# Optimization experiments

Hardware: AMD Instinct MI355X
Metric: run time of the kernel (lower is better)

Reference implementation:

```python
import jax, jax.numpy as jnp
import numpy as np

N = 50000
NEG_SLOPE = 0.2

def gat_conv(x, src, dst, W, a_src, a_dst, bias, heads, out_ch):
    # Linear projection per head: [N, H, C]
    h = (x @ W).reshape(x.shape[0], heads, out_ch)
    # Node-level attention terms alpha_src/alpha_dst: [N, H]
    al_src = jnp.einsum('nhc,hc->nh', h, a_src)
    al_dst = jnp.einsum('nhc,hc->nh', h, a_dst)
    # Edge logits with LeakyReLU: [E, H]
    logits = jax.nn.leaky_relu(al_src[src] + al_dst[dst], NEG_SLOPE)
    # Segment softmax over incoming edges of each dst node
    m = jax.ops.segment_max(logits, dst, num_segments=N)
    e = jnp.exp(logits - m[dst])
    s = jax.ops.segment_sum(e, dst, num_segments=N)
    alpha = e / (s[dst] + 1e-16)                      # [E, H]
    # Weighted message aggregation (scatter-add): [N, H, C]
    out = jax.ops.segment_sum(h[src] * alpha[..., None], dst, num_segments=N)
    return out.reshape(N, heads * out_ch) + bias


def setup_inputs() -> dict:
    key = jax.random.key(0)
    ks = jax.random.split(key, 12)
    in_ch, out_ch = 128, 256
    h1, c1 = 4, out_ch // 8          # conv1: 4 heads x 32
    mid = h1 * c1                    # 128 = out_ch // 2
    E = 1600000
    x = jax.random.normal(ks[0], (N, in_ch), jnp.float32)
    edge_index = jax.random.randint(ks[1], (2, E), 0, N, jnp.int64)
    sc = 0.1
    return {
        'x': x,
        'edge_index': edge_index,
        'W1': jax.random.normal(ks[2], (in_ch, h1 * c1), jnp.float32) * sc,
        'a_src1': jax.random.normal(ks[3], (h1, c1), jnp.float32) * sc,
        'a_dst1': jax.random.normal(ks[4], (h1, c1), jnp.float32) * sc,
        'b1': jnp.zeros((h1 * c1,), jnp.float32),
        'W2': jax.random.normal(ks[5], (mid, out_ch), jnp.float32) * sc,
        'a_src2': jax.random.normal(ks[6], (1, out_ch), jnp.float32) * sc,
        'a_dst2': jax.random.normal(ks[7], (1, out_ch), jnp.float32) * sc,
        'b2': jnp.zeros((out_ch,), jnp.float32),
    }


def reference(x, edge_index, W1, a_src1, a_dst1, b1, W2, a_src2, a_dst2, b2):
    # PyG GATConv adds self-loops by default
    loop = jnp.arange(N, dtype=edge_index.dtype)
    src = jnp.concatenate([edge_index[0], loop])
    dst = jnp.concatenate([edge_index[1], loop])
    h = gat_conv(x, src, dst, W1, a_src1, a_dst1, b1, heads=4, out_ch=32)
    h = jax.nn.relu(h)
    out = gat_conv(h, src, dst, W2, a_src2, a_dst2, b2, heads=1, out_ch=256)
    return out
```

## Files before the change

### kernel.cpp

```cpp
#include <hip/hip_runtime.h>
#include <hip/hip_fp16.h>
#include <math.h>

#define NSLOPE 0.2f
#define LOG2E  1.44269504f

typedef _Float16 half8 __attribute__((ext_vector_type(8)));
typedef float floatx4 __attribute__((ext_vector_type(4)));
typedef float floatx2 __attribute__((ext_vector_type(2)));

__device__ __forceinline__ float wcalc(float t) {
    float l = fmaxf(t, NSLOPE * t);
    float r;
    asm("v_exp_f32 %0, %1" : "=v"(r) : "v"(l));
    return r;
}

__device__ __forceinline__ void fma8_fp8(float* acc, float w, uint2 v) {
    floatx2 p0 = __builtin_amdgcn_cvt_pk_f32_fp8(v.x, false);
    floatx2 p1 = __builtin_amdgcn_cvt_pk_f32_fp8(v.x, true);
    floatx2 p2 = __builtin_amdgcn_cvt_pk_f32_fp8(v.y, false);
    floatx2 p3 = __builtin_amdgcn_cvt_pk_f32_fp8(v.y, true);
    acc[0] = fmaf(w, p0.x, acc[0]);
    acc[1] = fmaf(w, p0.y, acc[1]);
    acc[2] = fmaf(w, p1.x, acc[2]);
    acc[3] = fmaf(w, p1.y, acc[3]);
    acc[4] = fmaf(w, p2.x, acc[4]);
    acc[5] = fmaf(w, p2.y, acc[5]);
    acc[6] = fmaf(w, p3.x, acc[6]);
    acc[7] = fmaf(w, p3.y, acc[7]);
}

#define MAXB 5632
#define BE   8192

__global__ __launch_bounds__(256)
void prep_kernel(const int* __restrict__ dst, int* __restrict__ bcnt,
                 const float* __restrict__ x, __half* __restrict__ x16, int nx,
                 const float* __restrict__ W1, __half* __restrict__ W1T,
                 const float* __restrict__ W2, __half* __restrict__ W2T,
                 const float* __restrict__ a_src2, const float* __restrict__ a_dst2,
                 float* __restrict__ w2s, float* __restrict__ w2d,
                 int E, int Etot, int nb, int nbA, int ncast, int nt1, int nt2)
{
    __shared__ int hist[512];
    int bid = blockIdx.x;
    int tid = threadIdx.x;

    if (bid < nbA) {
        for (int i = tid; i < 512; i += 256) hist[i] = 0;
        __syncthreads();
        for (int e = bid * 256 + tid; e < Etot; e += nbA * 256) {
            int d = (e < E) ? dst[e] : (e - E);
            atomicAdd(&hist[d >> 7], 1);
        }
        __syncthreads();
        for (int i = tid; i < nb; i += 256) {
            int v = hist[i];
            if (v) atomicAdd(&bcnt[i], v);
        }
        return;
    }
    bid -= nbA;
    if (bid < ncast) {
        int i = (bid * 256 + tid) * 4;
        if (i < nx) {
            float4 v = *(const float4*)&x[i];
            __half2 a = __floats2half2_rn(v.x, v.y);
            __half2 b = __floats2half2_rn(v.z, v.w);
            *(uint2*)&x16[i] = make_uint2(*(unsigned*)&a, *(unsigned*)&b);
        }
        return;
    }
    bid -= ncast;
    if (bid < nt1) {
        int idx = bid * 256 + tid;
        int c = idx >> 7, k = idx & 127;
        W1T[(size_t)c * 128 + k] = __float2half(W1[(size_t)k * 128 + c]);
        return;
    }
    bid -= nt1;
    if (bid < nt2) {
        int idx = bid * 256 + tid;
        int c = idx >> 7, k = idx & 127;
        W2T[(size_t)c * 128 + k] = __float2half(W2[(size_t)k * 256 + c]);
        return;
    }
    {
        const float* a = (tid < 128) ? a_src2 : a_dst2;
        int k = tid & 127;
        float acc = 0.f;
        for (int c = 0; c < 256; c += 4) {
            float4 w = *(const float4*)&W2[(size_t)k * 256 + c];
            float4 av = *(const float4*)&a[c];
            acc = fmaf(w.x, av.x, fmaf(w.y, av.y, fmaf(w.z, av.z, fmaf(w.w, av.w, acc))));
        }
        if (tid < 128) w2s[k] = acc * LOG2E; else w2d[k] = acc * LOG2E;
    }
}

__global__ __launch_bounds__(512)
void scanBuckets_kernel(const int* __restrict__ bcnt, int* __restrict__ bbase,
                        int* __restrict__ gcur, int nb, int* __restrict__ offs,
                        int N, int total)
{
    __shared__ int tmp[512];
    int tid = threadIdx.x;
    int v = (tid < nb) ? bcnt[tid] : 0;
    tmp[tid] = v;
    __syncthreads();
    for (int off = 1; off < 512; off <<= 1) {
        int t = (tid >= off) ? tmp[tid - off] : 0;
        __syncthreads();
        tmp[tid] += t;
        __syncthreads();
    }
    if (tid < nb) {
        int e = tmp[tid] - v;
        bbase[tid] = e;
        gcur[tid] = e;
    }
    if (tid == 0) offs[N] = total;
}

__global__ __launch_bounds__(256)
void bucketB_kernel(const int* __restrict__ src, const int* __restrict__ dst,
                    int* __restrict__ gcur, unsigned* __restrict__ eout,
                    int E, int Etot, int nb)
{
    __shared__ int hist[512];
    __shared__ int res[512];
    __shared__ int lcur[512];
    int tid = threadIdx.x;
    int e0 = blockIdx.x * BE;
    int e1 = min(e0 + BE, Etot);

    for (int i = tid; i < 512; i += 256) hist[i] = 0;
    __syncthreads();
    for (int e = e0 + tid; e < e1; e += 256) {
        int d = (e < E) ? dst[e] : (e - E);
        atomicAdd(&hist[d >> 7], 1);
    }
    __syncthreads();
    for (int i = tid; i < nb; i += 256) {
        int h = hist[i];
        res[i] = h ? atomicAdd(&gcur[i], h) : 0;
        lcur[i] = 0;
    }
    __syncthreads();
    for (int e = e0 + tid; e < e1; e += 256) {
        int s, d;
        if (e < E) { s = src[e]; d = dst[e]; }
        else       { s = e - E; d = s; }
        int b = d >> 7;
        int p = res[b] + atomicAdd(&lcur[b], 1);
        eout[p] = (unsigned)s | ((unsigned)(d & 127) << 16);
    }
}

__global__ __launch_bounds__(256)
void combo_kernel(const unsigned* __restrict__ eout, const int* __restrict__ bbase,
                  const int* __restrict__ bcnt, unsigned short* __restrict__ csr,
                  int* __restrict__ offs, int N, int nb,
                  const __half* __restrict__ A16, const __half* __restrict__ W1T,
                  const float* __restrict__ a_src, const float* __restrict__ a_dst,
                  unsigned char* __restrict__ h1A, unsigned char* __restrict__ h1B,
                  float* __restrict__ al_src, float* __restrict__ al_dst)
{
    __shared__ unsigned eb[MAXB];
    __shared__ unsigned short sbuf[MAXB];
    __shared__ int cnt128[128], cur128[128], sc[128];

    int tid = threadIdx.x;
    if ((int)blockIdx.x < nb) {
        int b = blockIdx.x;
        int ebase = bbase[b];
        int ecnt = bcnt[b];
        int n0 = b << 7;
        int ncount = min(128, N - n0);

        if (tid < 128) cnt128[tid] = 0;
        for (int i = tid; i < ecnt; i += 256) eb[i] = eout[ebase + i];
        __syncthreads();
        for (int i = tid; i < ecnt; i += 256) atomicAdd(&cnt128[eb[i] >> 16], 1);
        __syncthreads();
        if (tid < 128) sc[tid] = cnt128[tid];
        __syncthreads();
        for (int off = 1; off < 128; off <<= 1) {
            int t = (tid >= off && tid < 128) ? sc[tid - off] : 0;
            __syncthreads();
            if (tid < 128) sc[tid] += t;
            __syncthreads();
        }
        if (tid < 128) {
            int excl = sc[tid] - cnt128[tid];
            cur128[tid] = excl;
            if (tid < ncount) offs[n0 + tid] = ebase + excl;
        }
        __syncthreads();
        for (int i = tid; i < ecnt; i += 256) {
            unsigned v = eb[i];
            int p = atomicAdd(&cur128[v >> 16], 1);
            sbuf[p] = (unsigned short)(v & 0xFFFFu);
        }
        __syncthreads();
        for (int i = tid; i < ecnt; i += 256) csr[ebase + i] = sbuf[i];
        return;
    }

    int gb = blockIdx.x - nb;
    int M = N;
    int wave = tid >> 6, lane = tid & 63;
    int lr = lane & 15, q = lane >> 4;
    int r0 = gb * 32 + (wave >> 1) * 16;
    int wcol = (wave & 1) * 64;
    unsigned char* hT = (wave & 1) ? h1B : h1A;

    int arow = min(r0 + lr, M - 1);
    const uint4* Arow = (const uint4*)A16 + (size_t)arow * 16;
    half8 a[4];
#pragma unroll
    for (int kb = 0; kb < 4; ++kb) {
        union { uint4 u; half8 h; } c;
        c.u = Arow[kb * 4 + q];
        a[kb] = c.h;
    }

    floatx4 acc[4];
    const floatx4 zero = {0.f, 0.f, 0.f, 0.f};
#pragma unroll
    for (int ct = 0; ct < 4; ++ct) acc[ct] = zero;

#pragma unroll
    for (int ct = 0; ct < 4; ++ct) {
        const uint4* Brow = (const uint4*)W1T + (size_t)(wcol + ct * 16 + lr) * 16;
#pragma unroll
        for (int kb = 0; kb < 4; ++kb) {
            union { uint4 u; half8 h; } c;
            c.u = Brow[kb * 4 + q];
            acc[ct] = __builtin_amdgcn_mfma_f32_16x16x32_f16(a[kb], c.h, acc[ct], 0, 0, 0);
        }
    }

#pragma unroll
    for (int ct = 0; ct < 4; ++ct) {
        int colh = ct * 16 + lr;
#pragma unroll
        for (int r = 0; r < 4; ++r) {
            int row = r0 + q * 4 + r;
            if (row < M) {
                unsigned pk = __builtin_amdgcn_cvt_pk_fp8_f32(acc[ct][r], acc[ct][r], 0, false);
                hT[(size_t)row * 64 + colh] = (unsigned char)(pk & 0xFF);
            }
        }
    }

    float as[4], ad[4];
#pragma unroll
    for (int ct = 0; ct < 4; ++ct) {
        int col = wcol + ct * 16 + lr;
        as[ct] = a_src[col] * LOG2E;
        ad[ct] = a_dst[col] * LOG2E;
    }
    int hb = wcol >> 5;
#pragma unroll
    for (int r = 0; r < 4; ++r) {
        float psA = acc[0][r] * as[0] + acc[1][r] * as[1];
        float psB = acc[2][r] * as[2] + acc[3][r] * as[3];
        float pdA = acc[0][r] * ad[0] + acc[1][r] * ad[1];
        float pdB = acc[2][r] * ad[2] + acc[3][r] * ad[3];
#pragma unroll
        for (int off = 1; off < 16; off <<= 1) {
            psA += __shfl_xor(psA, off); psB += __shfl_xor(psB, off);
            pdA += __shfl_xor(pdA, off); pdB += __shfl_xor(pdB, off);
        }
        if (lr == 0) {
            int row = r0 + q * 4 + r;
            if (row < M) {
                al_src[(size_t)row * 4 + hb]     = psA;
                al_src[(size_t)row * 4 + hb + 1] = psB;
                al_dst[(size_t)row * 4 + hb]     = pdA;
                al_dst[(size_t)row * 4 + hb + 1] = pdB;
            }
        }
    }
}

__global__ __launch_bounds__(256)
void gemm2_mfma(const __half* __restrict__ A16, const __half* __restrict__ W2T,
                const float* __restrict__ bias, float* __restrict__ out, int M)
{
    int wave = threadIdx.x >> 6, lane = threadIdx.x & 63;
    int lr = lane & 15, q = lane >> 4;
    int r0 = blockIdx.x * 16;
    int c0 = wave * 64;

    int arow = min(r0 + lr, M - 1);
    const uint4* Arow = (const uint4*)A16 + (size_t)arow * 16;
    half8 a[4];
#pragma unroll
    for (int kb = 0; kb < 4; ++kb) {
        union { uint4 u; half8 h; } c;
        c.u = Arow[kb * 4 + q];
        a[kb] = c.h;
    }

    floatx4 acc[4];
    const floatx4 zero = {0.f, 0.f, 0.f, 0.f};
#pragma unroll
    for (int ct = 0; ct < 4; ++ct) acc[ct] = zero;

#pragma unroll
    for (int ct = 0; ct < 4; ++ct) {
        const uint4* Brow = (const uint4*)W2T + (size_t)(c0 + ct * 16 + lr) * 16;
#pragma unroll
        for (int kb = 0; kb < 4; ++kb) {
            union { uint4 u; half8 h; } c;
            c.u = Brow[kb * 4 + q];
            acc[ct] = __builtin_amdgcn_mfma_f32_16x16x32_f16(a[kb], c.h, acc[ct], 0, 0, 0);
        }
    }

#pragma unroll
    for (int ct = 0; ct < 4; ++ct) {
        int col = c0 + ct * 16 + lr;
        float b = bias[col];
#pragma unroll
        for (int r = 0; r < 4; ++r) {
            int row = r0 + q * 4 + r;
            if (row < M) out[(size_t)row * 256 + col] = acc[ct][r] + b;
        }
    }
}

__global__ __launch_bounds__(256)
void agg1_half_kernel(const unsigned char* __restrict__ feat,
                      const unsigned short* __restrict__ csr_src,
                      const int* __restrict__ offs, const float* __restrict__ alS,
                      const float* __restrict__ alD, const float* __restrict__ bias,
                      const float* __restrict__ w2s, const float* __restrict__ w2d,
                      unsigned char* __restrict__ hmidH, float* __restrict__ alS2,
                      float* __restrict__ alD2, int N, int half)
{
    int lane = threadIdx.x & 63;
    int n = blockIdx.x * 4 + (threadIdx.x >> 6);
    if (n >= N) return;

    int lc = lane & 7;
    int es = lane >> 3;
    int head = half * 2 + (lc >> 2);

    float aD = alD[(size_t)n * 4 + head];
    int beg = offs[n], end = offs[n + 1];

    float acc0[8] = {0,0,0,0,0,0,0,0}, acc1[8] = {0,0,0,0,0,0,0,0};
    float sw0 = 0.f, sw1 = 0.f;
    const char* fbase = (const char*)feat + lc * 8;
    const float* alSh = alS + head;

    int j = beg + es;
    for (; j + 8 < end; j += 16) {
        int s0 = csr_src[j];
        int s1 = csr_src[j + 8];
        float w0 = wcalc(alSh[(size_t)s0 * 4] + aD);
        float w1 = wcalc(alSh[(size_t)s1 * 4] + aD);
        uint2 f0 = *(const uint2*)(fbase + (size_t)s0 * 64);
        uint2 f1 = *(const uint2*)(fbase + (size_t)s1 * 64);
        fma8_fp8(acc0, w0, f0); sw0 += w0;
        fma8_fp8(acc1, w1, f1); sw1 += w1;
    }
    if (j < end) {
        int s0 = csr_src[j];
        float w0 = wcalc(alSh[(size_t)s0 * 4] + aD);
        uint2 f0 = *(const uint2*)(fbase + (size_t)s0 * 64);
        fma8_fp8(acc0, w0, f0); sw0 += w0;
    }

    float sw = sw0 + sw1;
    sw += __shfl_xor(sw, 8); sw += __shfl_xor(sw, 16); sw += __shfl_xor(sw, 32);
#pragma unroll
    for (int i = 0; i < 8; ++i) {
        acc0[i] += acc1[i];
        acc0[i] += __shfl_xor(acc0[i], 8);
        acc0[i] += __shfl_xor(acc0[i], 16);
        acc0[i] += __shfl_xor(acc0[i], 32);
    }

    if (lane < 8) {
        float inv = 1.f / (sw + 1e-16f);
        int cb = half * 64 + lc * 8;
        float v[8];
#pragma unroll
        for (int i = 0; i < 8; ++i)
            v[i] = fmaxf(fmaf(acc0[i], inv, bias[cb + i]), 0.f);
        unsigned pk0 = __builtin_amdgcn_cvt_pk_fp8_f32(v[0], v[1], 0, false);
        pk0 = __builtin_amdgcn_cvt_pk_fp8_f32(v[2], v[3], pk0, true);
        unsigned pk1 = __builtin_amdgcn_cvt_pk_fp8_f32(v[4], v[5], 0, false);
        pk1 = __builtin_amdgcn_cvt_pk_fp8_f32(v[6], v[7], pk1, true);
        ((uint2*)hmidH)[(size_t)n * 8 + lc] = make_uint2(pk0, pk1);
        float ps = 0.f, pd = 0.f;
#pragma unroll
        for (int i = 0; i < 8; ++i) {
            ps = fmaf(v[i], w2s[cb + i], ps);
            pd = fmaf(v[i], w2d[cb + i], pd);
        }
        ps += __shfl_xor(ps, 1); ps += __shfl_xor(ps, 2); ps += __shfl_xor(ps, 4);
        pd += __shfl_xor(pd, 1); pd += __shfl_xor(pd, 2); pd += __shfl_xor(pd, 4);
        if (lane == 0) {
            if (half == 0) { alS2[n] = ps;          alD2[n] = pd; }
            else           { alS2[n] = alS2[n] + ps; alD2[n] = alD2[n] + pd; }
        }
    }
}

__global__ __launch_bounds__(256)
void agg2_half_kernel(const unsigned char* __restrict__ feat,
                      const unsigned short* __restrict__ csr_src,
                      const int* __restrict__ offs, const float* __restrict__ alS,
                      const float* __restrict__ alD, __half* __restrict__ m16,
                      int N, int half)
{
    int lane = threadIdx.x & 63;
    int n = blockIdx.x * 4 + (threadIdx.x >> 6);
    if (n >= N) return;

    int lc = lane & 7;
    int es = lane >> 3;

    float aD = alD[n];
    int beg = offs[n], end = offs[n + 1];

    float acc0[8] = {0,0,0,0,0,0,0,0}, acc1[8] = {0,0,0,0,0,0,0,0};
    float sw0 = 0.f, sw1 = 0.f;
    const char* fbase = (const char*)feat + lc * 8;

    int j = beg + es;
    for (; j + 8 < end; j += 16) {
        int s0 = csr_src[j];
        int s1 = csr_src[j + 8];
        float w0 = wcalc(alS[s0] + aD);
        float w1 = wcalc(alS[s1] + aD);
        uint2 f0 = *(const uint2*)(fbase + (size_t)s0 * 64);
        uint2 f1 = *(const uint2*)(fbase + (size_t)s1 * 64);
        fma8_fp8(acc0, w0, f0); sw0 += w0;
        fma8_fp8(acc1, w1, f1); sw1 += w1;
    }
    if (j < end) {
        int s0 = csr_src[j];
        float w0 = wcalc(alS[s0] + aD);
        uint2 f0 = *(const uint2*)(fbase + (size_t)s0 * 64);
        fma8_fp8(acc0, w0, f0); sw0 += w0;
    }

    float sw = sw0 + sw1;
    sw += __shfl_xor(sw, 8); sw += __shfl_xor(sw, 16); sw += __shfl_xor(sw, 32);
#pragma unroll
    for (int i = 0; i < 8; ++i) {
        acc0[i] += acc1[i];
        acc0[i] += __shfl_xor(acc0[i], 8);
        acc0[i] += __shfl_xor(acc0[i], 16);
        acc0[i] += __shfl_xor(acc0[i], 32);
    }

    if (lane < 8) {
        float inv = 1.f / (sw + 1e-16f);
        float v[8];
#pragma unroll
        for (int i = 0; i < 8; ++i) v[i] = acc0[i] * inv;
        __half2 p0 = __floats2half2_rn(v[0], v[1]);
        __half2 p1 = __floats2half2_rn(v[2], v[3]);
        __half2 p2 = __floats2half2_rn(v[4], v[5]);
        __half2 p3 = __floats2half2_rn(v[6], v[7]);
        uint4 pk = make_uint4(*(unsigned*)&p0, *(unsigned*)&p1,
                              *(unsigned*)&p2, *(unsigned*)&p3);
        ((uint4*)m16)[(size_t)n * 16 + half * 8 + lc] = pk;
    }
}

extern "C" void kernel_launch(void* const* d_in, const int* in_sizes, int n_in,
                              void* d_out, int out_size, void* d_ws, size_t ws_size,
                              hipStream_t stream)
{
    const float* x      = (const float*)d_in[0];
    const int*   ei     = (const int*)d_in[1];
    const float* W1     = (const float*)d_in[2];
    const float* a_src1 = (const float*)d_in[3];
    const float* a_dst1 = (const float*)d_in[4];
    const float* b1     = (const float*)d_in[5];
    const float* W2     = (const float*)d_in[6];
    const float* a_src2 = (const float*)d_in[7];
    const float* a_dst2 = (const float*)d_in[8];
    const float* b2     = (const float*)d_in[9];

    const int N    = in_sizes[0] / 128;
    const int E    = in_sizes[1] / 2;
    const int Etot = E + N;
    const int* src = ei;
    const int* dst = ei + E;
    const int nb   = (N + 127) >> 7;

    char* ws = (char*)d_ws;
    size_t off = 0;
    auto carve = [&](size_t bytes) -> void* {
        void* p = ws + off;
        off += (bytes + 255) & ~(size_t)255;
        return p;
    };
    __half*  x16  = (__half*)carve((size_t)N * 128 * 2);
    unsigned char* h1A   = (unsigned char*)carve((size_t)N * 64);
    unsigned char* h1B   = (unsigned char*)carve((size_t)N * 64);
    unsigned char* hmidA = (unsigned char*)carve((size_t)N * 64);
    unsigned char* hmidB = (unsigned char*)carve((size_t)N * 64);
    __half*  m16  = (__half*)carve((size_t)N * 128 * 2);
    __half*  W1T  = (__half*)carve(128 * 128 * 2);
    __half*  W2T  = (__half*)carve(256 * 128 * 2);
    float*   alS1 = (float*)carve((size_t)N * 4 * 4);
    float*   alD1 = (float*)carve((size_t)N * 4 * 4);
    float*   alS2 = (float*)carve((size_t)N * 4);
    float*   alD2 = (float*)carve((size_t)N * 4);
    float*   w2s  = (float*)carve(128 * 4);
    float*   w2d  = (float*)carve(128 * 4);
    int*     offs = (int*)carve((size_t)(N + 1) * 4);
    int*     bcnt = (int*)carve(512 * 4);
    int*     bbas = (int*)carve(512 * 4);
    int*     gcur = (int*)carve(512 * 4);
    unsigned* eout = (unsigned*)carve((size_t)Etot * 4);
    unsigned short* csr = (unsigned short*)carve((size_t)Etot * 2);
    (void)ws_size; (void)n_in; (void)out_size;

    const int TB = 256;
    const int agrid = (N + 3) / 4;
    const int g1grid = (N + 31) / 32;
    const int g2grid = (N + 15) / 16;
    const int nx = N * 128;

    const int nbA   = 512;
    const int ncast = (nx / 4 + TB - 1) / TB;
    const int nt1   = (128 * 128 + TB - 1) / TB;
    const int nt2   = (256 * 128 + TB - 1) / TB;
    const int nprep = nbA + ncast + nt1 + nt2 + 1;

    hipMemsetAsync(bcnt, 0, 512 * 4, stream);

    prep_kernel<<<nprep, TB, 0, stream>>>(dst, bcnt, x, x16, nx, W1, W1T, W2, W2T,
                                          a_src2, a_dst2, w2s, w2d,
                                          E, Etot, nb, nbA, ncast, nt1, nt2);
    scanBuckets_kernel<<<1, 512, 0, stream>>>(bcnt, bbas, gcur, nb, offs, N, Etot);
    bucketB_kernel<<<(Etot + BE - 1) / BE, TB, 0, stream>>>(src, dst, gcur, eout, E, Etot, nb);
    combo_kernel<<<nb + g1grid, TB, 0, stream>>>(eout, bbas, bcnt, csr, offs, N, nb,
                                                 x16, W1T, a_src1, a_dst1, h1A, h1B, alS1, alD1);
    agg1_half_kernel<<<agrid, TB, 0, stream>>>(h1A, csr, offs, alS1, alD1, b1,
                                               w2s, w2d, hmidA, alS2, alD2, N, 0);
    agg1_half_kernel<<<agrid, TB, 0, stream>>>(h1B, csr, offs, alS1, alD1, b1,
                                               w2s, w2d, hmidB, alS2, alD2, N, 1);
    agg2_half_kernel<<<agrid, TB, 0, stream>>>(hmidA, csr, offs, alS2, alD2, m16, N, 0);
    agg2_half_kernel<<<agrid, TB, 0, stream>>>(hmidB, csr, offs, alS2, alD2, m16, N, 1);
    gemm2_mfma<<<g2grid, TB, 0, stream>>>(m16, W2T, b2, (float*)d_out, N);
}
```

Before: 336.8 us.

## Merge half-split fp8 feature buffers and aggregate full rows in one pass

Replaces the two half-width fp8 feature buffers (64 bytes per node) with single 128-byte rows. Each aggregation layer now runs as one kernel instead of two, with each lane loading 16 bytes per edge and accumulating with packed FMA. This halves the number of times the CSR, offsets and attention scalars are traversed and removes the read-modify-write of alS2/alD2 across halves. In exchange it uses more accumulator registers per lane, which may lower occupancy, and issues wider gathers.

```diff
diff --git a/kernel.cpp b/kernel.cpp
--- a/kernel.cpp
+++ b/kernel.cpp
@@ -16,19 +16,16 @@
     return r;
 }
 
-__device__ __forceinline__ void fma8_fp8(float* acc, float w, uint2 v) {
-    floatx2 p0 = __builtin_amdgcn_cvt_pk_f32_fp8(v.x, false);
-    floatx2 p1 = __builtin_amdgcn_cvt_pk_f32_fp8(v.x, true);
-    floatx2 p2 = __builtin_amdgcn_cvt_pk_f32_fp8(v.y, false);
-    floatx2 p3 = __builtin_amdgcn_cvt_pk_f32_fp8(v.y, true);
-    acc[0] = fmaf(w, p0.x, acc[0]);
-    acc[1] = fmaf(w, p0.y, acc[1]);
-    acc[2] = fmaf(w, p1.x, acc[2]);
-    acc[3] = fmaf(w, p1.y, acc[3]);
-    acc[4] = fmaf(w, p2.x, acc[4]);
-    acc[5] = fmaf(w, p2.y, acc[5]);
-    acc[6] = fmaf(w, p3.x, acc[6]);
-    acc[7] = fmaf(w, p3.y, acc[7]);
+__device__ __forceinline__ void fma16_fp8(floatx2* acc, float w, uint4 v) {
+    floatx2 ww; ww.x = w; ww.y = w;
+    unsigned u[4] = {v.x, v.y, v.z, v.w};
+#pragma unroll
+    for (int i = 0; i < 4; ++i) {
+        floatx2 lo = __builtin_amdgcn_cvt_pk_f32_fp8(u[i], false);
+        floatx2 hi = __builtin_amdgcn_cvt_pk_f32_fp8(u[i], true);
+        asm("v_pk_fma_f32 %0, %1, %2, %0" : "+v"(acc[2 * i])     : "v"(lo), "v"(ww));
+        asm("v_pk_fma_f32 %0, %1, %2, %0" : "+v"(acc[2 * i + 1]) : "v"(hi), "v"(ww));
+    }
 }
 
 #define MAXB 5632
@@ -164,8 +161,8 @@
                   int* __restrict__ offs, int N, int nb,
                   const __half* __restrict__ A16, const __half* __restrict__ W1T,
                   const float* __restrict__ a_src, const float* __restrict__ a_dst,
-                  unsigned char* __restrict__ h1A, unsigned char* __restrict__ h1B,
-                  float* __restrict__ al_src, float* __restrict__ al_dst)
+                  unsigned char* __restrict__ h1, float* __restrict__ al_src,
+                  float* __restrict__ al_dst)
 {
     __shared__ unsigned eb[MAXB];
     __shared__ unsigned short sbuf[MAXB];
@@ -214,7 +211,6 @@
     int lr = lane & 15, q = lane >> 4;
     int r0 = gb * 32 + (wave >> 1) * 16;
     int wcol = (wave & 1) * 64;
-    unsigned char* hT = (wave & 1) ? h1B : h1A;
 
     int arow = min(r0 + lr, M - 1);
     const uint4* Arow = (const uint4*)A16 + (size_t)arow * 16;
@@ -244,13 +240,13 @@
 
 #pragma unroll
     for (int ct = 0; ct < 4; ++ct) {
-        int colh = ct * 16 + lr;
+        int col = wcol + ct * 16 + lr;
 #pragma unroll
         for (int r = 0; r < 4; ++r) {
             int row = r0 + q * 4 + r;
             if (row < M) {
                 unsigned pk = __builtin_amdgcn_cvt_pk_fp8_f32(acc[ct][r], acc[ct][r], 0, false);
-                hT[(size_t)row * 64 + colh] = (unsigned char)(pk & 0xFF);
+                h1[(size_t)row * 128 + col] = (unsigned char)(pk & 0xFF);
             }
         }
     }
@@ -334,13 +330,12 @@
 }
 
 __global__ __launch_bounds__(256)
-void agg1_half_kernel(const unsigned char* __restrict__ feat,
-                      const unsigned short* __restrict__ csr_src,
-                      const int* __restrict__ offs, const float* __restrict__ alS,
-                      const float* __restrict__ alD, const float* __restrict__ bias,
-                      const float* __restrict__ w2s, const float* __restrict__ w2d,
-                      unsigned char* __restrict__ hmidH, float* __restrict__ alS2,
-                      float* __restrict__ alD2, int N, int half)
+void agg1_kernel(const unsigned char* __restrict__ feat, const unsigned short* __restrict__ csr_src,
+                 const int* __restrict__ offs, const float* __restrict__ alS,
+                 const float* __restrict__ alD, const float* __restrict__ bias,
+                 const float* __restrict__ w2s, const float* __restrict__ w2d,
+                 unsigned char* __restrict__ hmid, float* __restrict__ alS2,
+                 float* __restrict__ alD2, int N)
 {
     int lane = threadIdx.x & 63;
     int n = blockIdx.x * 4 + (threadIdx.x >> 6);
@@ -348,77 +343,79 @@
 
     int lc = lane & 7;
     int es = lane >> 3;
-    int head = half * 2 + (lc >> 2);
-
-    float aD = alD[(size_t)n * 4 + head];
+    int head = lc >> 1;
+    unsigned lcoff = (unsigned)(lc * 16);
+
+    float aD = alD[(unsigned)(n << 2) + head];
     int beg = offs[n], end = offs[n + 1];
 
-    float acc0[8] = {0,0,0,0,0,0,0,0}, acc1[8] = {0,0,0,0,0,0,0,0};
+    floatx2 acc0[8], acc1[8];
+    floatx2 zz; zz.x = 0.f; zz.y = 0.f;
+#pragma unroll
+    for (int i = 0; i < 8; ++i) { acc0[i] = zz; acc1[i] = zz; }
     float sw0 = 0.f, sw1 = 0.f;
-    const char* fbase = (const char*)feat + lc * 8;
-    const float* alSh = alS + head;
 
     int j = beg + es;
     for (; j + 8 < end; j += 16) {
         int s0 = csr_src[j];
         int s1 = csr_src[j + 8];
-        float w0 = wcalc(alSh[(size_t)s0 * 4] + aD);
-        float w1 = wcalc(alSh[(size_t)s1 * 4] + aD);
-        uint2 f0 = *(const uint2*)(fbase + (size_t)s0 * 64);
-        uint2 f1 = *(const uint2*)(fbase + (size_t)s1 * 64);
-        fma8_fp8(acc0, w0, f0); sw0 += w0;
-        fma8_fp8(acc1, w1, f1); sw1 += w1;
+        float w0 = wcalc(alS[(unsigned)(s0 << 2) + head] + aD);
+        float w1 = wcalc(alS[(unsigned)(s1 << 2) + head] + aD);
+        uint4 f0 = *(const uint4*)(feat + ((unsigned)(s0 << 7) + lcoff));
+        uint4 f1 = *(const uint4*)(feat + ((unsigned)(s1 << 7) + lcoff));
+        fma16_fp8(acc0, w0, f0); sw0 += w0;
+        fma16_fp8(acc1, w1, f1); sw1 += w1;
     }
     if (j < end) {
         int s0 = csr_src[j];
-        float w0 = wcalc(alSh[(size_t)s0 * 4] + aD);
-        uint2 f0 = *(const uint2*)(fbase + (size_t)s0 * 64);
-        fma8_fp8(acc0, w0, f0); sw0 += w0;
+        float w0 = wcalc(alS[(unsigned)(s0 << 2) + head] + aD);
+        uint4 f0 = *(const uint4*)(feat + ((unsigned)(s0 << 7) + lcoff));
+        fma16_fp8(acc0, w0, f0); sw0 += w0;
     }
 
     float sw = sw0 + sw1;
     sw += __shfl_xor(sw, 8); sw += __shfl_xor(sw, 16); sw += __shfl_xor(sw, 32);
+    float v[16];
 #pragma unroll
     for (int i = 0; i < 8; ++i) {
-        acc0[i] += acc1[i];
-        acc0[i] += __shfl_xor(acc0[i], 8);
-        acc0[i] += __shfl_xor(acc0[i], 16);
-        acc0[i] += __shfl_xor(acc0[i], 32);
-    }
-
+        float e0 = acc0[i].x + acc1[i].x;
+        float e1 = acc0[i].y + acc1[i].y;
+        e0 += __shfl_xor(e0, 8); e0 += __shfl_xor(e0, 16); e0 += __shfl_xor(e0, 32);
+        e1 += __shfl_xor(e1, 8); e1 += __shfl_xor(e1, 16); e1 += __shfl_xor(e1, 32);
+        v[2 * i] = e0; v[2 * i + 1] = e1;
+    }
+
+    float ps = 0.f, pd = 0.f;
     if (lane < 8) {
         float inv = 1.f / (sw + 1e-16f);
-        int cb = half * 64 + lc * 8;
-        float v[8];
-#pragma unroll
-        for (int i = 0; i < 8; ++i)
-            v[i] = fmaxf(fmaf(acc0[i], inv, bias[cb + i]), 0.f);
-        unsigned pk0 = __builtin_amdgcn_cvt_pk_fp8_f32(v[0], v[1], 0, false);
-        pk0 = __builtin_amdgcn_cvt_pk_fp8_f32(v[2], v[3], pk0, true);
-        unsigned pk1 = __builtin_amdgcn_cvt_pk_fp8_f32(v[4], v[5], 0, false);
-        pk1 = __builtin_amdgcn_cvt_pk_fp8_f32(v[6], v[7], pk1, true);
-        ((uint2*)hmidH)[(size_t)n * 8 + lc] = make_uint2(pk0, pk1);
-        float ps = 0.f, pd = 0.f;
-#pragma unroll
-        for (int i = 0; i < 8; ++i) {
+        int cb = lc * 16;
+#pragma unroll
+        for (int i = 0; i < 16; ++i)
+            v[i] = fmaxf(fmaf(v[i], inv, bias[cb + i]), 0.f);
+        unsigned q0 = __builtin_amdgcn_cvt_pk_fp8_f32(v[0],  v[1],  0, false);
+        q0 = __builtin_amdgcn_cvt_pk_fp8_f32(v[2],  v[3],  q0, true);
+        unsigned q1 = __builtin_amdgcn_cvt_pk_fp8_f32(v[4],  v[5],  0, false);
+        q1 = __builtin_amdgcn_cvt_pk_fp8_f32(v[6],  v[7],  q1, true);
+        unsigned q2 = __builtin_amdgcn_cvt_pk_fp8_f32(v[8],  v[9],  0, false);
+        q2 = __builtin_amdgcn_cvt_pk_fp8_f32(v[10], v[11], q2, true);
+        unsigned q3 = __builtin_amdgcn_cvt_pk_fp8_f32(v[12], v[13], 0, false);
+        q3 = __builtin_amdgcn_cvt_pk_fp8_f32(v[14], v[15], q3, true);
+        ((uint4*)hmid)[(size_t)n * 8 + lc] = make_uint4(q0, q1, q2, q3);
+#pragma unroll
+        for (int i = 0; i < 16; ++i) {
             ps = fmaf(v[i], w2s[cb + i], ps);
             pd = fmaf(v[i], w2d[cb + i], pd);
         }
-        ps += __shfl_xor(ps, 1); ps += __shfl_xor(ps, 2); ps += __shfl_xor(ps, 4);
-        pd += __shfl_xor(pd, 1); pd += __shfl_xor(pd, 2); pd += __shfl_xor(pd, 4);
-        if (lane == 0) {
-            if (half == 0) { alS2[n] = ps;          alD2[n] = pd; }
-            else           { alS2[n] = alS2[n] + ps; alD2[n] = alD2[n] + pd; }
-        }
-    }
+    }
+    ps += __shfl_xor(ps, 1); ps += __shfl_xor(ps, 2); ps += __shfl_xor(ps, 4);
+    pd += __shfl_xor(pd, 1); pd += __shfl_xor(pd, 2); pd += __shfl_xor(pd, 4);
+    if (lane == 0) { alS2[n] = ps; alD2[n] = pd; }
 }
 
 __global__ __launch_bounds__(256)
-void agg2_half_kernel(const unsigned char* __restrict__ feat,
-                      const unsigned short* __restrict__ csr_src,
-                      const int* __restrict__ offs, const float* __restrict__ alS,
-                      const float* __restrict__ alD, __half* __restrict__ m16,
-                      int N, int half)
+void agg2_kernel(const unsigned char* __restrict__ feat, const unsigned short* __restrict__ csr_src,
+                 const int* __restrict__ offs, const float* __restrict__ alS,
+                 const float* __restrict__ alD, __half* __restrict__ m16, int N)
 {
     int lane = threadIdx.x & 63;
     int n = blockIdx.x * 4 + (threadIdx.x >> 6);
@@ -426,13 +423,16 @@
 
     int lc = lane & 7;
     int es = lane >> 3;
+    unsigned lcoff = (unsigned)(lc * 16);
 
     float aD = alD[n];
     int beg = offs[n], end = offs[n + 1];
 
-    float acc0[8] = {0,0,0,0,0,0,0,0}, acc1[8] = {0,0,0,0,0,0,0,0};
+    floatx2 acc0[8], acc1[8];
+    floatx2 zz; zz.x = 0.f; zz.y = 0.f;
+#pragma unroll
+    for (int i = 0; i < 8; ++i) { acc0[i] = zz; acc1[i] = zz; }
     float sw0 = 0.f, sw1 = 0.f;
-    const char* fbase = (const char*)feat + lc * 8;
 
     int j = beg + es;
     for (; j + 8 < end; j += 16) {
@@ -440,40 +440,42 @@
         int s1 = csr_src[j + 8];
         float w0 = wcalc(alS[s0] + aD);
         float w1 = wcalc(alS[s1] + aD);
-        uint2 f0 = *(const uint2*)(fbase + (size_t)s0 * 64);
-        uint2 f1 = *(const uint2*)(fbase + (size_t)s1 * 64);
-        fma8_fp8(acc0, w0, f0); sw0 += w0;
-        fma8_fp8(acc1, w1, f1); sw1 += w1;
+        uint4 f0 = *(const uint4*)(feat + ((unsigned)(s0 << 7) + lcoff));
+        uint4 f1 = *(const uint4*)(feat + ((unsigned)(s1 << 7) + lcoff));
+        fma16_fp8(acc0, w0, f0); sw0 += w0;
+        fma16_fp8(acc1, w1, f1); sw1 += w1;
     }
     if (j < end) {
         int s0 = csr_src[j];
         float w0 = wcalc(alS[s0] + aD);
-        uint2 f0 = *(const uint2*)(fbase + (size_t)s0 * 64);
-        fma8_fp8(acc0, w0, f0); sw0 += w0;
+        uint4 f0 = *(const uint4*)(feat + ((unsigned)(s0 << 7) + lcoff));
+        fma16_fp8(acc0, w0, f0); sw0 += w0;
     }
 
     float sw = sw0 + sw1;
     sw += __shfl_xor(sw, 8); sw += __shfl_xor(sw, 16); sw += __shfl_xor(sw, 32);
+    float v[16];
 #pragma unroll
     for (int i = 0; i < 8; ++i) {
-        acc0[i] += acc1[i];
-        acc0[i] += __shfl_xor(acc0[i], 8);
-        acc0[i] += __shfl_xor(acc0[i], 16);
-        acc0[i] += __shfl_xor(acc0[i], 32);
+        float e0 = acc0[i].x + acc1[i].x;
+        float e1 = acc0[i].y + acc1[i].y;
+        e0 += __shfl_xor(e0, 8); e0 += __shfl_xor(e0, 16); e0 += __shfl_xor(e0, 32);
+        e1 += __shfl_xor(e1, 8); e1 += __shfl_xor(e1, 16); e1 += __shfl_xor(e1, 32);
+        v[2 * i] = e0; v[2 * i + 1] = e1;
     }
 
     if (lane < 8) {
         float inv = 1.f / (sw + 1e-16f);
-        float v[8];
-#pragma unroll
-        for (int i = 0; i < 8; ++i) v[i] = acc0[i] * inv;
-        __half2 p0 = __floats2half2_rn(v[0], v[1]);
-        __half2 p1 = __floats2half2_rn(v[2], v[3]);
-        __half2 p2 = __floats2half2_rn(v[4], v[5]);
-        __half2 p3 = __floats2half2_rn(v[6], v[7]);
-        uint4 pk = make_uint4(*(unsigned*)&p0, *(unsigned*)&p1,
-                              *(unsigned*)&p2, *(unsigned*)&p3);
-        ((uint4*)m16)[(size_t)n * 16 + half * 8 + lc] = pk;
+        __half2 p[8];
+#pragma unroll
+        for (int i = 0; i < 8; ++i)
+            p[i] = __floats2half2_rn(v[2 * i] * inv, v[2 * i + 1] * inv);
+        uint4 pk0 = make_uint4(*(unsigned*)&p[0], *(unsigned*)&p[1],
+                               *(unsigned*)&p[2], *(unsigned*)&p[3]);
+        uint4 pk1 = make_uint4(*(unsigned*)&p[4], *(unsigned*)&p[5],
+                               *(unsigned*)&p[6], *(unsigned*)&p[7]);
+        ((uint4*)m16)[(size_t)n * 16 + lc * 2]     = pk0;
+        ((uint4*)m16)[(size_t)n * 16 + lc * 2 + 1] = pk1;
     }
 }
 
@@ -507,10 +509,8 @@
         return p;
     };
     __half*  x16  = (__half*)carve((size_t)N * 128 * 2);
-    unsigned char* h1A   = (unsigned char*)carve((size_t)N * 64);
-    unsigned char* h1B   = (unsigned char*)carve((size_t)N * 64);
-    unsigned char* hmidA = (unsigned char*)carve((size_t)N * 64);
-    unsigned char* hmidB = (unsigned char*)carve((size_t)N * 64);
+    unsigned char* h1   = (unsigned char*)carve((size_t)N * 128);
+    unsigned char* hmid = (unsigned char*)carve((size_t)N * 128);
     __half*  m16  = (__half*)carve((size_t)N * 128 * 2);
     __half*  W1T  = (__half*)carve(128 * 128 * 2);
     __half*  W2T  = (__half*)carve(256 * 128 * 2);
@@ -548,12 +548,9 @@
     scanBuckets_kernel<<<1, 512, 0, stream>>>(bcnt, bbas, gcur, nb, offs, N, Etot);
     bucketB_kernel<<<(Etot + BE - 1) / BE, TB, 0, stream>>>(src, dst, gcur, eout, E, Etot, nb);
     combo_kernel<<<nb + g1grid, TB, 0, stream>>>(eout, bbas, bcnt, csr, offs, N, nb,
-                                                 x16, W1T, a_src1, a_dst1, h1A, h1B, alS1, alD1);
-    agg1_half_kernel<<<agrid, TB, 0, stream>>>(h1A, csr, offs, alS1, alD1, b1,
-                                               w2s, w2d, hmidA, alS2, alD2, N, 0);
-    agg1_half_kernel<<<agrid, TB, 0, stream>>>(h1B, csr, offs, alS1, alD1, b1,
-                                               w2s, w2d, hmidB, alS2, alD2, N, 1);
-    agg2_half_kernel<<<agrid, TB, 0, stream>>>(hmidA, csr, offs, alS2, alD2, m16, N, 0);
-    agg2_half_kernel<<<agrid, TB, 0, stream>>>(hmidB, csr, offs, alS2, alD2, m16, N, 1);
+                                                 x16, W1T, a_src1, a_dst1, h1, alS1, alD1);
+    agg1_kernel<<<agrid, TB, 0, stream>>>(h1, csr, offs, alS1, alD1, b1,
+                                          w2s, w2d, hmid, alS2, alD2, N);
+    agg2_kernel<<<agrid, TB, 0, stream>>>(hmid, csr, offs, alS2, alD2, m16, N);
     gemm2_mfma<<<g2grid, TB, 0, stream>>>(m16, W2T, b2, (float*)d_out, N);
 }
```

New measurement: 305.6 us. 9.2% less time.
